# Kernel tuning notes

Measured on AMD Instinct MI355X. Metric: run time of the kernel, lower is better.

The kernel has to match this reference:

```python
import jax, jax.numpy as jnp
import numpy as np

N_NODES = 10000
N_EDGES = 160000
C = 16        # num_feature_channels
C2 = 8        # output channels per irrep per head (C/2)
HID = 64      # radial_network_hidden_units
NH = 2        # num_attention_heads
NG = 16       # graphs in batch
F_IN = 64     # num_features
F_OUT = 32    # number_of_output_features
HEAD_TYPES = ("normal", "inverse")  # invariant_dictionary
IRREP_SLICES = ((0, 1), (1, 4), (4, 9))  # l=0,1,2 blocks of the SH dim


def _sph_harm(r):
    """Component-normalized real spherical harmonics l=0..2 for unit vectors r [E,3] -> [E,9]."""
    x, y, z = r[:, 0], r[:, 1], r[:, 2]
    c3 = 1.7320508   # sqrt(3)
    c15 = 3.8729833  # sqrt(15)
    l0 = jnp.ones_like(x)[:, None]
    l1 = c3 * r
    l2 = jnp.stack([
        c15 * x * y,
        c15 * y * z,
        1.1180340 * (2.0 * z * z - x * x - y * y),  # sqrt(5)/2
        c15 * x * z,
        1.9364917 * (x * x - y * y),                 # sqrt(15)/2
    ], axis=-1)
    return jnp.concatenate([l0, l1, l2], axis=-1)


def setup_inputs() -> dict:
    key = jax.random.key(0)
    ks = jax.random.split(key, 16)
    node_features = jax.random.normal(ks[0], (N_NODES, F_IN), jnp.float32)
    pos = jax.random.normal(ks[1], (N_NODES, 3), jnp.float32)
    src = jax.random.randint(ks[2], (N_EDGES,), 0, N_NODES)
    off = jax.random.randint(ks[3], (N_EDGES,), 1, N_NODES)  # avoid self-loops (d=0)
    tgt = (src + off) % N_NODES
    edge_index = jnp.stack([src, tgt], axis=0)
    batch = jnp.sort(jax.random.randint(ks[4], (N_NODES,), 0, NG))
    s = lambda k, shape, fan: (jax.random.normal(k, shape, jnp.float32) / np.sqrt(fan)).astype(jnp.float32)
    return dict(
        node_features=node_features, pos=pos,
        W_embed=s(ks[5], (F_IN, C), F_IN), b_embed=jnp.zeros((C,), jnp.float32),
        Wq=s(ks[6], (NH, C, C), C), Wk=s(ks[7], (NH, C, C), C),
        W1=s(ks[8], (NH, 1, HID), 1), b1=jnp.zeros((NH, HID), jnp.float32),
        Wa=s(ks[9], (NH, HID), HID), Wv=s(ks[10], (NH, HID, C * 3), HID),
        Wo=s(ks[11], (NH, 3, C, C2), C),
        Wproj=s(ks[12], (NH * C2, F_OUT), NH * C2), bproj=jnp.zeros((F_OUT,), jnp.float32),
        edge_index=edge_index, batch=batch,
    )


def _forward(node_features, pos, W_embed, b_embed, Wq, Wk, W1, b1, Wa, Wv, Wo,
             Wproj, bproj, edge_index, batch):
    src, tgt = edge_index[0], edge_index[1]
    rel = pos[tgt] - pos[src]                       # [E,3]
    dist = jnp.linalg.norm(rel, axis=-1, keepdims=True)  # [E,1]
    rhat = rel / dist
    Y = _sph_harm(rhat)                             # [E,9]
    x = node_features @ W_embed + b_embed          # [N,C] scalar (0e) features
    xs = x[src]                                     # [E,C]
    inv_sqrt_c = 1.0 / np.sqrt(C)
    head_outs = []
    for h in range(NH):
        d_feat = dist if HEAD_TYPES[h] == "normal" else dist ** -2  # [E,1]
        hid = jax.nn.relu(d_feat @ W1[h] + b1[h])   # [E,HID] radial network
        att_bias = hid @ Wa[h]                      # [E]
        wv = (hid @ Wv[h]).reshape(-1, C, 3)        # [E,C,3] per-(channel,l) radial weights
        q = x @ Wq[h]
        k = x @ Wk[h]
        logit = jnp.sum(q[tgt] * k[src], axis=-1) * inv_sqrt_c + att_bias  # [E]
        # segment softmax over incoming edges of each target node
        m = jax.ops.segment_max(logit, tgt, num_segments=N_NODES)
        e = jnp.exp(logit - m[tgt])
        z = jax.ops.segment_sum(e, tgt, num_segments=N_NODES)
        alpha = e / z[tgt]                          # [E]
        # expand per-l weights to per-m: dims (1,3,5)
        wv_m = jnp.repeat(wv, np.array([1, 3, 5]), axis=2, total_repeat_length=9)  # [E,C,9]
        msg = (alpha[:, None, None] * wv_m) * xs[:, :, None] * Y[:, None, :]       # [E,C,9]
        node_out = jax.ops.segment_sum(msg, tgt, num_segments=N_NODES)             # [N,C,9]
        parts = [jnp.einsum('ncm,co->nom', node_out[:, :, s0:s1], Wo[h, li]).reshape(N_NODES, -1)
                 for li, (s0, s1) in enumerate(IRREP_SLICES)]
        head_outs.append(jnp.concatenate(parts, axis=-1))  # [N, C2*9]
    feat = jnp.concatenate(head_outs, axis=-1)              # [N, NH*C2*9]
    pooled = jax.ops.segment_sum(feat, batch, num_segments=NG)  # [NG, NH*C2*9]
    # equivariant Linear -> F_OUT x 0e: only scalar (l=0) components map to scalars
    blk = C2 * 9
    scal = jnp.concatenate([pooled[:, h * blk: h * blk + C2] for h in range(NH)], axis=-1)  # [NG, NH*C2]
    return scal @ Wproj + bproj                             # [NG, F_OUT]


def reference(node_features, pos, W_embed, b_embed, Wq, Wk, W1, b1, Wa, Wv, Wo,
              Wproj, bproj, edge_index, batch):
    return _forward(node_features, pos, W_embed, b_embed, Wq, Wk, W1, b1, Wa, Wv,
                    Wo, Wproj, bproj, edge_index, batch)
```

## Files before the change

### kernel.cpp

```cpp
#include <hip/hip_runtime.h>
#include <math.h>

#define NN 10000
#define NE 160000
#define CAP 96
#define TPH 2432
#define AATT_OFF 64
#define BATT_OFF 132
#define A_OFF 200
#define B_OFF 1312


__device__ __forceinline__ unsigned bf16pack2(float a, float b) {
    unsigned ua = __float_as_uint(a);
    unsigned ub = __float_as_uint(b);
    ua = ua + 0x7fffu + ((ua >> 16) & 1u);
    ub = ub + 0x7fffu + ((ub >> 16) & 1u);
    return (ua >> 16) | (ub & 0xffff0000u);
}

__global__ __launch_bounds__(256) void k_xqk(const float* __restrict__ nf,
        const float* __restrict__ We, const float* __restrict__ be,
        const float* __restrict__ Wq, const float* __restrict__ Wk,
        const float* __restrict__ W1, const float* __restrict__ b1,
        const float* __restrict__ Wa, const float* __restrict__ Wv,
        float* __restrict__ x, float* __restrict__ q, float* __restrict__ k,
        int* __restrict__ zeroReg, float* __restrict__ tab) {
    int t = threadIdx.x;
    int gid = blockIdx.x * 256 + t;
    if (gid < 10256) zeroReg[gid] = 0;
    __shared__ float sWe[64 * 16];
    __shared__ float sWq[2 * 16 * 16];
    __shared__ float sWk[2 * 16 * 16];
    __shared__ float sNF[16 * 64];
    __shared__ float sX[16 * 16];
    __shared__ float sT[2][64], sDA[2][64], sDB[2][64], sIA[2][64], sIB[2][64];
    __shared__ float sW[2][64][17];
    __shared__ short sOrd[2][64];
    for (int i = t; i < 1024; i += 256) sWe[i] = We[i];
    for (int i = t; i < 512; i += 256) { sWq[i] = Wq[i]; sWk[i] = Wk[i]; }
    int nodeBase = blockIdx.x * 16;
    for (int i = t; i < 1024; i += 256) {
        int n = nodeBase + (i >> 6);
        sNF[i] = (n < NN) ? nf[n * 64 + (i & 63)] : 0.0f;
    }
    __syncthreads();
    int ln = t >> 4, c = t & 15;
    int n = nodeBase + ln;
    float acc = be[c];
    #pragma unroll 16
    for (int j = 0; j < 64; ++j) acc = fmaf(sNF[ln * 64 + j], sWe[j * 16 + c], acc);
    sX[ln * 16 + c] = acc;
    __syncthreads();
    if (n < NN) {
        x[n * 16 + c] = acc;
        #pragma unroll
        for (int h = 0; h < 2; ++h) {
            float aq = 0.0f, ak = 0.0f;
            #pragma unroll
            for (int j = 0; j < 16; ++j) {
                float xv = sX[ln * 16 + j];
                aq = fmaf(xv, sWq[(h * 16 + j) * 16 + c], aq);
                ak = fmaf(xv, sWk[(h * 16 + j) * 16 + c], ak);
            }
            q[(n * 2 + h) * 16 + c] = aq;
            k[(n * 2 + h) * 16 + c] = ak;
        }
    }
    if (blockIdx.x == 0) {
        if (t < 128) {
            int h = t >> 6, j = t & 63;
            float a = W1[h * 64 + j], b = b1[h * 64 + j];
            float da = 0.0f, db = 0.0f, ia = 0.0f, ib = 0.0f, th;
            if (a > 0.0f)      { th = -b / a; da = a;  db = b; }
            else if (a < 0.0f) { th = -b / a; da = -a; db = -b; ia = a; ib = b; }
            else               { th = INFINITY; if (b > 0.0f) ib = b; }
            sT[h][j] = th; sDA[h][j] = da; sDB[h][j] = db; sIA[h][j] = ia; sIB[h][j] = ib;
        }
        for (int i = t; i < 2 * 64 * 17; i += 256) {
            int h = i / 1088, r = i % 1088, j = r / 17, cc = r % 17;
            sW[h][j][cc] = (cc < 16) ? Wv[(h * 64 + j) * 48 + 3 * cc] : Wa[h * 64 + j];
        }
        __syncthreads();
        if (t < 128) {
            int h = t >> 6, j = t & 63;
            float tj = sT[h][j];
            int r = 0;
            #pragma unroll 16
            for (int kk = 0; kk < 64; ++kk) {
                float tk = sT[h][kk];
                r += (tk < tj || (tk == tj && kk < j)) ? 1 : 0;
            }
            sOrd[h][r] = (short)j;
            tab[h * TPH + r] = tj;
        }
        __syncthreads();
        if (t < 34) {
            int h = t / 17, cc = t % 17;
            float A = 0.0f, B = 0.0f;
            #pragma unroll 8
            for (int j = 0; j < 64; ++j) {
                float w = sW[h][j][cc];
                A = fmaf(sIA[h][j], w, A);
                B = fmaf(sIB[h][j], w, B);
            }
            float* pa; float* pb; int stride;
            if (cc == 16) { pa = tab + h * TPH + AATT_OFF; pb = tab + h * TPH + BATT_OFF; stride = 1; }
            else          { pa = tab + h * TPH + A_OFF + cc; pb = tab + h * TPH + B_OFF + cc; stride = 17; }
            pa[0] = A; pb[0] = B;
            #pragma unroll 8
            for (int sg = 1; sg <= 64; ++sg) {
                int u = sOrd[h][sg - 1];
                float w = sW[h][u][cc];
                A = fmaf(sDA[h][u], w, A);
                B = fmaf(sDB[h][u], w, B);
                pa[sg * stride] = A;
                pb[sg * stride] = B;
            }
        }
    }
}

__global__ __launch_bounds__(256) void k_edge(const float* __restrict__ pos,
        const int* __restrict__ ei,
        const float* __restrict__ q, const float* __restrict__ k,
        const float* __restrict__ Wo, const float* __restrict__ x,
        const float* __restrict__ tab, int* __restrict__ deg,
        float* __restrict__ lgp, uint4* __restrict__ gb) {
    __shared__ float sTab[2 * TPH];
    int tid = threadIdx.x;
    for (int i = tid; i < 2 * TPH; i += 256) sTab[i] = tab[i];
    __syncthreads();
    int e = blockIdx.x * 256 + tid;
    if (e >= NE) return;
    int s = ei[e], t = ei[NE + e];
    int p = atomicAdd(&deg[t], 1);
    bool ok = (p < CAP);
    size_t slot = (size_t)t * CAP + p;
    float dx = pos[t * 3 + 0] - pos[s * 3 + 0];
    float dy = pos[t * 3 + 1] - pos[s * 3 + 1];
    float dz = pos[t * 3 + 2] - pos[s * 3 + 2];
    float d = sqrtf(dx * dx + dy * dy + dz * dz);
    float fh2[2] = { d, 1.0f / (d * d) };
    const float4* xp = (const float4*)(x + (size_t)s * 16);
    float4 xs0 = xp[0], xs1 = xp[1], xs2 = xp[2], xs3 = xp[3];
    float xf[16] = { xs0.x, xs0.y, xs0.z, xs0.w, xs1.x, xs1.y, xs1.z, xs1.w,
                     xs2.x, xs2.y, xs2.z, xs2.w, xs3.x, xs3.y, xs3.z, xs3.w };
    float L2v[2];
    #pragma unroll
    for (int h = 0; h < 2; ++h) {
        const float4* qt = (const float4*)(q + (size_t)t * 32 + h * 16);
        const float4* ks = (const float4*)(k + (size_t)s * 32 + h * 16);
        float4 a0 = qt[0], a1 = qt[1], a2 = qt[2], a3 = qt[3];
        float4 b0 = ks[0], c1 = ks[1], c2 = ks[2], c3 = ks[3];
        float dot = a0.x * b0.x + a0.y * b0.y + a0.z * b0.z + a0.w * b0.w
                  + a1.x * c1.x + a1.y * c1.y + a1.z * c1.z + a1.w * c1.w
                  + a2.x * c2.x + a2.y * c2.y + a2.z * c2.z + a2.w * c2.w
                  + a3.x * c3.x + a3.y * c3.y + a3.z * c3.z + a3.w * c3.w;
        float f = fh2[h];
        const float* tb = sTab + h * TPH;
        int sg = 0;
        #pragma unroll
        for (int st = 32; st >= 1; st >>= 1)
            if (tb[sg + st - 1] < f) sg += st;
        if (tb[sg] < f) ++sg;
        float att = fmaf(tb[AATT_OFF + sg], f, tb[BATT_OFF + sg]);
        L2v[h] = fmaf(dot, 0.25f, att);
        const float* Ab = tb + A_OFF + sg * 17;
        const float* Bb = tb + B_OFF + sg * 17;
        const float* wob = Wo + h * 384;
        float g[8];
        #pragma unroll
        for (int o = 0; o < 8; ++o) g[o] = 0.0f;
        #pragma unroll
        for (int c = 0; c < 16; ++c) {
            float axc = fmaf(Ab[c], f, Bb[c]) * xf[c];
            #pragma unroll
            for (int o = 0; o < 8; ++o) g[o] = fmaf(axc, wob[c * 8 + o], g[o]);
        }
        if (ok) {
            gb[slot * 2 + h] = make_uint4(bf16pack2(g[0], g[1]), bf16pack2(g[2], g[3]),
                                          bf16pack2(g[4], g[5]), bf16pack2(g[6], g[7]));
        }
    }
    if (ok) *(float2*)(lgp + slot * 2) = make_float2(L2v[0], L2v[1]);
}

__global__ __launch_bounds__(256) void k_gather(const int* __restrict__ deg,
        const float* __restrict__ lgp, const unsigned* __restrict__ gb,
        float* __restrict__ feat) {
    int t0 = threadIdx.x;
    int wv = t0 >> 6;
    int lane = t0 & 63;
    int pid = blockIdx.x * 4 + wv;
    int n = pid >> 1, h = pid & 1;
    int dg = min(deg[n], CAP);
    int g = lane >> 2, p = lane & 3;
    float m = -INFINITY, z = 0.0f, u0 = 0.0f, u1 = 0.0f;
    const float* lgb = lgp + (size_t)n * (CAP * 2) + h;
    const unsigned* gbb = gb + (size_t)n * (CAP * 8) + h * 4 + p;
    for (int i = g; i < dg; i += 16) {
        float L = lgb[i * 2];
        unsigned wbits = gbb[(size_t)i * 8];
        float ga = __uint_as_float(wbits << 16);
        float gbv = __uint_as_float(wbits & 0xffff0000u);
        float nm = fmaxf(m, L);
        float sc = (m > -INFINITY) ? __expf(m - nm) : 0.0f;
        float w  = __expf(L - nm);
        u0 = fmaf(u0, sc, w * ga);
        u1 = fmaf(u1, sc, w * gbv);
        z  = fmaf(z, sc, w);
        m = nm;
    }
    #pragma unroll
    for (int off = 4; off <= 32; off <<= 1) {
        float mo = __shfl_xor(m, off, 64);
        float zo = __shfl_xor(z, off, 64);
        float a0o = __shfl_xor(u0, off, 64);
        float a1o = __shfl_xor(u1, off, 64);
        float nm = fmaxf(m, mo);
        float a = (m  > -INFINITY) ? __expf(m  - nm) : 0.0f;
        float b = (mo > -INFINITY) ? __expf(mo - nm) : 0.0f;
        u0 = u0 * a + a0o * b;
        u1 = u1 * a + a1o * b;
        z  = z * a + zo * b;
        m = nm;
    }
    if (lane < 4) {
        float inv = (z > 0.0f) ? 1.0f / z : 0.0f;
        *(float2*)(feat + n * 16 + h * 8 + p * 2) = make_float2(u0 * inv, u1 * inv);
    }
}

__global__ __launch_bounds__(256) void k_pool(const float* __restrict__ feat,
        const int* __restrict__ batch, float* __restrict__ pooled) {
    __shared__ float sP[256];
    int t = threadIdx.x;
    sP[t] = 0.0f;
    __syncthreads();
    int tid = blockIdx.x * 256 + t;
    int c = tid & 15, seg = tid >> 4;
    int n0 = seg * 16, n1 = min(n0 + 16, NN);
    float run = 0.0f;
    int curg = -1;
    for (int n = n0; n < n1; ++n) {
        int gg = batch[n];
        if (gg != curg) {
            if (curg >= 0) atomicAdd(&sP[curg * 16 + c], run);
            run = 0.0f; curg = gg;
        }
        run += feat[n * 16 + c];
    }
    if (curg >= 0) atomicAdd(&sP[curg * 16 + c], run);
    __syncthreads();
    atomicAdd(&pooled[t], sP[t]);
}

__global__ __launch_bounds__(512) void k_final(const float* __restrict__ pooled,
        const float* __restrict__ Wproj, const float* __restrict__ bproj,
        float* __restrict__ out) {
    int t = threadIdx.x;
    int g = t >> 5, fo = t & 31;
    float acc = bproj[fo];
    #pragma unroll
    for (int j = 0; j < 16; ++j) acc = fmaf(pooled[g * 16 + j], Wproj[j * 32 + fo], acc);
    out[g * 32 + fo] = acc;
}

extern "C" void kernel_launch(void* const* d_in, const int* in_sizes, int n_in,
                              void* d_out, int out_size, void* d_ws, size_t ws_size,
                              hipStream_t stream) {
    const float* nf    = (const float*)d_in[0];
    const float* pos   = (const float*)d_in[1];
    const float* We    = (const float*)d_in[2];
    const float* be    = (const float*)d_in[3];
    const float* Wq    = (const float*)d_in[4];
    const float* Wk    = (const float*)d_in[5];
    const float* W1    = (const float*)d_in[6];
    const float* b1    = (const float*)d_in[7];
    const float* Wa    = (const float*)d_in[8];
    const float* Wv    = (const float*)d_in[9];
    const float* Wo    = (const float*)d_in[10];
    const float* Wproj = (const float*)d_in[11];
    const float* bproj = (const float*)d_in[12];
    const int*   ei    = (const int*)d_in[13];
    const int*   batch = (const int*)d_in[14];
    float* out = (float*)d_out;
    (void)in_sizes; (void)n_in; (void)out_size; (void)ws_size;

    float* ws     = (float*)d_ws;
    float* x      = ws;
    float* q      = x + 160000;
    float* k      = q + 320000;
    float* feat   = k + 320000;
    float* pooled = feat + 160000;
    int*   deg    = (int*)(pooled + 256);
    float* tab    = (float*)(deg + 10000);
    float* lgp    = tab + 4864;
    unsigned* gbu = (unsigned*)(lgp + (size_t)NN * CAP * 2);

    hipLaunchKernelGGL(k_xqk,    dim3(625),  dim3(256), 0, stream, nf, We, be, Wq, Wk, W1, b1, Wa, Wv, x, q, k, (int*)pooled, tab);
    hipLaunchKernelGGL(k_edge,   dim3(625),  dim3(256), 0, stream, pos, ei, q, k, Wo, x, tab, deg, lgp, (uint4*)gbu);
    hipLaunchKernelGGL(k_gather, dim3(5000), dim3(256), 0, stream, deg, lgp, gbu, feat);
    hipLaunchKernelGGL(k_pool,   dim3(40),   dim3(256), 0, stream, feat, batch, pooled);
    hipLaunchKernelGGL(k_final,  dim3(1),    dim3(512), 0, stream, pooled, Wproj, bproj, out);
}
```

Baseline: 138.9 us.

## Bin edges by target in prep, compute messages per node with online softmax

Edge binning by target now happens in the first kernel, which stores only source indices. A new per-node kernel (32 lanes per node) computes the distances, table lookups, messages and online softmax directly, then combines lanes with shuffles. This replaces the separate edge kernel that wrote bf16 messages and logits, and the gather kernel that read them back, removing a large intermediate round trip. Pool and final projection are merged using a last-block counter, the table build is parallelised with prefix sums, and the A/B rows are padded to 20 for float4 loads. In exchange, the table is now read from global memory rather than LDS, and work per wave is uneven across lanes for nodes with low degree.

```diff
diff --git a/kernel.cpp b/kernel.cpp
--- a/kernel.cpp
+++ b/kernel.cpp
@@ -4,39 +4,33 @@
 #define NN 10000
 #define NE 160000
 #define CAP 96
-#define TPH 2432
+#define TPH 2832
 #define AATT_OFF 64
 #define BATT_OFF 132
 #define A_OFF 200
-#define B_OFF 1312
-
-
-__device__ __forceinline__ unsigned bf16pack2(float a, float b) {
-    unsigned ua = __float_as_uint(a);
-    unsigned ub = __float_as_uint(b);
-    ua = ua + 0x7fffu + ((ua >> 16) & 1u);
-    ub = ub + 0x7fffu + ((ub >> 16) & 1u);
-    return (ua >> 16) | (ub & 0xffff0000u);
-}
-
-__global__ __launch_bounds__(256) void k_xqk(const float* __restrict__ nf,
+#define B_OFF 1520
+
+
+__global__ __launch_bounds__(256) void k_pre(const float* __restrict__ nf,
         const float* __restrict__ We, const float* __restrict__ be,
         const float* __restrict__ Wq, const float* __restrict__ Wk,
         const float* __restrict__ W1, const float* __restrict__ b1,
         const float* __restrict__ Wa, const float* __restrict__ Wv,
+        const int* __restrict__ ei,
         float* __restrict__ x, float* __restrict__ q, float* __restrict__ k,
-        int* __restrict__ zeroReg, float* __restrict__ tab) {
+        int* __restrict__ deg, int* __restrict__ srcBin, float* __restrict__ tab) {
     int t = threadIdx.x;
     int gid = blockIdx.x * 256 + t;
-    if (gid < 10256) zeroReg[gid] = 0;
+    {
+        int s = ei[gid], tt = ei[NE + gid];
+        int p = atomicAdd(&deg[tt], 1);
+        if (p < CAP) srcBin[tt * CAP + p] = s;
+    }
     __shared__ float sWe[64 * 16];
     __shared__ float sWq[2 * 16 * 16];
     __shared__ float sWk[2 * 16 * 16];
     __shared__ float sNF[16 * 64];
     __shared__ float sX[16 * 16];
-    __shared__ float sT[2][64], sDA[2][64], sDB[2][64], sIA[2][64], sIB[2][64];
-    __shared__ float sW[2][64][17];
-    __shared__ short sOrd[2][64];
     for (int i = t; i < 1024; i += 256) sWe[i] = We[i];
     for (int i = t; i < 512; i += 256) { sWq[i] = Wq[i]; sWk[i] = Wk[i]; }
     int nodeBase = blockIdx.x * 16;
@@ -68,6 +62,10 @@
         }
     }
     if (blockIdx.x == 0) {
+        __shared__ float sT[2][64], sDA[2][64], sDB[2][64], sIA[2][64], sIB[2][64];
+        __shared__ float sW[2][64][17];
+        __shared__ short sOrd[2][64];
+        __shared__ float sQA[2][17][4], sQB[2][17][4], sPA[2][17][4], sPB[2][17][4];
         if (t < 128) {
             int h = t >> 6, j = t & 63;
             float a = W1[h * 64 + j], b = b1[h * 64 + j];
@@ -95,145 +93,155 @@
             tab[h * TPH + r] = tj;
         }
         __syncthreads();
-        if (t < 34) {
-            int h = t / 17, cc = t % 17;
-            float A = 0.0f, B = 0.0f;
-            #pragma unroll 8
-            for (int j = 0; j < 64; ++j) {
-                float w = sW[h][j][cc];
-                A = fmaf(sIA[h][j], w, A);
-                B = fmaf(sIB[h][j], w, B);
-            }
+        int h = 0, cc = 0, qt = 0;
+        bool act = (t < 136);
+        if (act) { h = t / 68; int r = t % 68; cc = r >> 2; qt = r & 3; }
+        float qsA = 0.f, qsB = 0.f, ipA = 0.f, ipB = 0.f;
+        if (act) {
+            #pragma unroll 4
+            for (int i = 0; i < 16; ++i) {
+                int r = qt * 16 + i;
+                int u = sOrd[h][r];
+                float w = sW[h][u][cc];
+                qsA = fmaf(sDA[h][u], w, qsA);
+                qsB = fmaf(sDB[h][u], w, qsB);
+                float wj = sW[h][r][cc];
+                ipA = fmaf(sIA[h][r], wj, ipA);
+                ipB = fmaf(sIB[h][r], wj, ipB);
+            }
+            sQA[h][cc][qt] = qsA; sQB[h][cc][qt] = qsB;
+            sPA[h][cc][qt] = ipA; sPB[h][cc][qt] = ipB;
+        }
+        __syncthreads();
+        if (act) {
+            float A = sPA[h][cc][0] + sPA[h][cc][1] + sPA[h][cc][2] + sPA[h][cc][3];
+            float B = sPB[h][cc][0] + sPB[h][cc][1] + sPB[h][cc][2] + sPB[h][cc][3];
+            for (int qq = 0; qq < qt; ++qq) { A += sQA[h][cc][qq]; B += sQB[h][cc][qq]; }
             float* pa; float* pb; int stride;
             if (cc == 16) { pa = tab + h * TPH + AATT_OFF; pb = tab + h * TPH + BATT_OFF; stride = 1; }
-            else          { pa = tab + h * TPH + A_OFF + cc; pb = tab + h * TPH + B_OFF + cc; stride = 17; }
-            pa[0] = A; pb[0] = B;
-            #pragma unroll 8
-            for (int sg = 1; sg <= 64; ++sg) {
-                int u = sOrd[h][sg - 1];
+            else          { pa = tab + h * TPH + A_OFF + cc; pb = tab + h * TPH + B_OFF + cc; stride = 20; }
+            #pragma unroll 4
+            for (int i = 0; i < 16; ++i) {
+                int r = qt * 16 + i;
+                pa[r * stride] = A;
+                pb[r * stride] = B;
+                int u = sOrd[h][r];
                 float w = sW[h][u][cc];
                 A = fmaf(sDA[h][u], w, A);
                 B = fmaf(sDB[h][u], w, B);
-                pa[sg * stride] = A;
-                pb[sg * stride] = B;
-            }
+            }
+            if (qt == 3) { pa[64 * stride] = A; pb[64 * stride] = B; }
         }
     }
 }
 
-__global__ __launch_bounds__(256) void k_edge(const float* __restrict__ pos,
-        const int* __restrict__ ei,
-        const float* __restrict__ q, const float* __restrict__ k,
-        const float* __restrict__ Wo, const float* __restrict__ x,
-        const float* __restrict__ tab, int* __restrict__ deg,
-        float* __restrict__ lgp, uint4* __restrict__ gb) {
-    __shared__ float sTab[2 * TPH];
-    int tid = threadIdx.x;
-    for (int i = tid; i < 2 * TPH; i += 256) sTab[i] = tab[i];
-    __syncthreads();
-    int e = blockIdx.x * 256 + tid;
-    if (e >= NE) return;
-    int s = ei[e], t = ei[NE + e];
-    int p = atomicAdd(&deg[t], 1);
-    bool ok = (p < CAP);
-    size_t slot = (size_t)t * CAP + p;
-    float dx = pos[t * 3 + 0] - pos[s * 3 + 0];
-    float dy = pos[t * 3 + 1] - pos[s * 3 + 1];
-    float dz = pos[t * 3 + 2] - pos[s * 3 + 2];
-    float d = sqrtf(dx * dx + dy * dy + dz * dz);
-    float fh2[2] = { d, 1.0f / (d * d) };
-    const float4* xp = (const float4*)(x + (size_t)s * 16);
-    float4 xs0 = xp[0], xs1 = xp[1], xs2 = xp[2], xs3 = xp[3];
-    float xf[16] = { xs0.x, xs0.y, xs0.z, xs0.w, xs1.x, xs1.y, xs1.z, xs1.w,
-                     xs2.x, xs2.y, xs2.z, xs2.w, xs3.x, xs3.y, xs3.z, xs3.w };
-    float L2v[2];
+__global__ __launch_bounds__(256) void k_node(const float* __restrict__ pos,
+        const int* __restrict__ deg, const int* __restrict__ srcBin,
+        const float* __restrict__ q, const float* __restrict__ kk,
+        const float* __restrict__ x, const float* __restrict__ tab,
+        const float* __restrict__ Wo, float* __restrict__ feat) {
+    int t = threadIdx.x;
+    int n = blockIdx.x * 8 + (t >> 5);
+    int lane = t & 31;
+    int dg = min(deg[n], CAP);
+    float ptx = pos[n * 3 + 0], pty = pos[n * 3 + 1], ptz = pos[n * 3 + 2];
+    const float4* qp = (const float4*)(q + (size_t)n * 32);
+    float4 qv0 = qp[0], qv1 = qp[1], qv2 = qp[2], qv3 = qp[3];
+    float4 qv4 = qp[4], qv5 = qp[5], qv6 = qp[6], qv7 = qp[7];
+    float m[2] = { -INFINITY, -INFINITY };
+    float z[2] = { 0.0f, 0.0f };
+    float u[2][8];
+    #pragma unroll
+    for (int h = 0; h < 2; ++h)
+        #pragma unroll
+        for (int o = 0; o < 8; ++o) u[h][o] = 0.0f;
+    for (int slot = lane; slot < dg; slot += 32) {
+        int s = srcBin[n * CAP + slot];
+        float dx = ptx - pos[s * 3 + 0];
+        float dy = pty - pos[s * 3 + 1];
+        float dz = ptz - pos[s * 3 + 2];
+        float d = sqrtf(dx * dx + dy * dy + dz * dz);
+        const float4* xp = (const float4*)(x + (size_t)s * 16);
+        float4 xs0 = xp[0], xs1 = xp[1], xs2 = xp[2], xs3 = xp[3];
+        float Xf[16] = { xs0.x, xs0.y, xs0.z, xs0.w, xs1.x, xs1.y, xs1.z, xs1.w,
+                         xs2.x, xs2.y, xs2.z, xs2.w, xs3.x, xs3.y, xs3.z, xs3.w };
+        #pragma unroll
+        for (int h = 0; h < 2; ++h) {
+            const float4* kp = (const float4*)(kk + (size_t)s * 32 + h * 16);
+            float4 k0 = kp[0], k1 = kp[1], k2 = kp[2], k3 = kp[3];
+            float4 a0 = h ? qv4 : qv0, a1 = h ? qv5 : qv1;
+            float4 a2 = h ? qv6 : qv2, a3 = h ? qv7 : qv3;
+            float dot = a0.x * k0.x + a0.y * k0.y + a0.z * k0.z + a0.w * k0.w
+                      + a1.x * k1.x + a1.y * k1.y + a1.z * k1.z + a1.w * k1.w
+                      + a2.x * k2.x + a2.y * k2.y + a2.z * k2.z + a2.w * k2.w
+                      + a3.x * k3.x + a3.y * k3.y + a3.z * k3.z + a3.w * k3.w;
+            float f = h ? 1.0f / (d * d) : d;
+            const float* tb = tab + h * TPH;
+            int sg = 0;
+            #pragma unroll
+            for (int st = 32; st >= 1; st >>= 1)
+                if (tb[sg + st - 1] < f) sg += st;
+            if (tb[sg] < f) ++sg;
+            float att = fmaf(tb[AATT_OFF + sg], f, tb[BATT_OFF + sg]);
+            float L = fmaf(dot, 0.25f, att);
+            const float4* Ar = (const float4*)(tb + A_OFF + sg * 20);
+            const float4* Br = (const float4*)(tb + B_OFF + sg * 20);
+            float4 A0 = Ar[0], A1 = Ar[1], A2 = Ar[2], A3 = Ar[3];
+            float4 B0 = Br[0], B1 = Br[1], B2 = Br[2], B3 = Br[3];
+            float Af[16] = { A0.x, A0.y, A0.z, A0.w, A1.x, A1.y, A1.z, A1.w,
+                             A2.x, A2.y, A2.z, A2.w, A3.x, A3.y, A3.z, A3.w };
+            float Bf[16] = { B0.x, B0.y, B0.z, B0.w, B1.x, B1.y, B1.z, B1.w,
+                             B2.x, B2.y, B2.z, B2.w, B3.x, B3.y, B3.z, B3.w };
+            float g[8];
+            #pragma unroll
+            for (int o = 0; o < 8; ++o) g[o] = 0.0f;
+            const float* wob = Wo + h * 384;
+            #pragma unroll
+            for (int c = 0; c < 16; ++c) {
+                float ax = fmaf(Af[c], f, Bf[c]) * Xf[c];
+                #pragma unroll
+                for (int o = 0; o < 8; ++o) g[o] = fmaf(ax, wob[c * 8 + o], g[o]);
+            }
+            float nm = fmaxf(m[h], L);
+            float sc = (m[h] > -INFINITY) ? __expf(m[h] - nm) : 0.0f;
+            float w = __expf(L - nm);
+            #pragma unroll
+            for (int o = 0; o < 8; ++o) u[h][o] = fmaf(u[h][o], sc, w * g[o]);
+            z[h] = fmaf(z[h], sc, w);
+            m[h] = nm;
+        }
+    }
     #pragma unroll
     for (int h = 0; h < 2; ++h) {
-        const float4* qt = (const float4*)(q + (size_t)t * 32 + h * 16);
-        const float4* ks = (const float4*)(k + (size_t)s * 32 + h * 16);
-        float4 a0 = qt[0], a1 = qt[1], a2 = qt[2], a3 = qt[3];
-        float4 b0 = ks[0], c1 = ks[1], c2 = ks[2], c3 = ks[3];
-        float dot = a0.x * b0.x + a0.y * b0.y + a0.z * b0.z + a0.w * b0.w
-                  + a1.x * c1.x + a1.y * c1.y + a1.z * c1.z + a1.w * c1.w
-                  + a2.x * c2.x + a2.y * c2.y + a2.z * c2.z + a2.w * c2.w
-                  + a3.x * c3.x + a3.y * c3.y + a3.z * c3.z + a3.w * c3.w;
-        float f = fh2[h];
-        const float* tb = sTab + h * TPH;
-        int sg = 0;
-        #pragma unroll
-        for (int st = 32; st >= 1; st >>= 1)
-            if (tb[sg + st - 1] < f) sg += st;
-        if (tb[sg] < f) ++sg;
-        float att = fmaf(tb[AATT_OFF + sg], f, tb[BATT_OFF + sg]);
-        L2v[h] = fmaf(dot, 0.25f, att);
-        const float* Ab = tb + A_OFF + sg * 17;
-        const float* Bb = tb + B_OFF + sg * 17;
-        const float* wob = Wo + h * 384;
-        float g[8];
-        #pragma unroll
-        for (int o = 0; o < 8; ++o) g[o] = 0.0f;
-        #pragma unroll
-        for (int c = 0; c < 16; ++c) {
-            float axc = fmaf(Ab[c], f, Bb[c]) * xf[c];
-            #pragma unroll
-            for (int o = 0; o < 8; ++o) g[o] = fmaf(axc, wob[c * 8 + o], g[o]);
-        }
-        if (ok) {
-            gb[slot * 2 + h] = make_uint4(bf16pack2(g[0], g[1]), bf16pack2(g[2], g[3]),
-                                          bf16pack2(g[4], g[5]), bf16pack2(g[6], g[7]));
-        }
-    }
-    if (ok) *(float2*)(lgp + slot * 2) = make_float2(L2v[0], L2v[1]);
+        float mh = m[h], zh = z[h];
+        #pragma unroll
+        for (int off = 1; off <= 16; off <<= 1) {
+            float mo = __shfl_xor(mh, off, 64);
+            float zo = __shfl_xor(zh, off, 64);
+            float uo[8];
+            #pragma unroll
+            for (int o = 0; o < 8; ++o) uo[o] = __shfl_xor(u[h][o], off, 64);
+            float nm = fmaxf(mh, mo);
+            float a = (mh > -INFINITY) ? __expf(mh - nm) : 0.0f;
+            float b = (mo > -INFINITY) ? __expf(mo - nm) : 0.0f;
+            #pragma unroll
+            for (int o = 0; o < 8; ++o) u[h][o] = u[h][o] * a + uo[o] * b;
+            zh = zh * a + zo * b;
+            mh = nm;
+        }
+        if (lane == 0) {
+            float inv = (zh > 0.0f) ? 1.0f / zh : 0.0f;
+            float4* fp = (float4*)(feat + (size_t)n * 16 + h * 8);
+            fp[0] = make_float4(u[h][0] * inv, u[h][1] * inv, u[h][2] * inv, u[h][3] * inv);
+            fp[1] = make_float4(u[h][4] * inv, u[h][5] * inv, u[h][6] * inv, u[h][7] * inv);
+        }
+    }
 }
 
-__global__ __launch_bounds__(256) void k_gather(const int* __restrict__ deg,
-        const float* __restrict__ lgp, const unsigned* __restrict__ gb,
-        float* __restrict__ feat) {
-    int t0 = threadIdx.x;
-    int wv = t0 >> 6;
-    int lane = t0 & 63;
-    int pid = blockIdx.x * 4 + wv;
-    int n = pid >> 1, h = pid & 1;
-    int dg = min(deg[n], CAP);
-    int g = lane >> 2, p = lane & 3;
-    float m = -INFINITY, z = 0.0f, u0 = 0.0f, u1 = 0.0f;
-    const float* lgb = lgp + (size_t)n * (CAP * 2) + h;
-    const unsigned* gbb = gb + (size_t)n * (CAP * 8) + h * 4 + p;
-    for (int i = g; i < dg; i += 16) {
-        float L = lgb[i * 2];
-        unsigned wbits = gbb[(size_t)i * 8];
-        float ga = __uint_as_float(wbits << 16);
-        float gbv = __uint_as_float(wbits & 0xffff0000u);
-        float nm = fmaxf(m, L);
-        float sc = (m > -INFINITY) ? __expf(m - nm) : 0.0f;
-        float w  = __expf(L - nm);
-        u0 = fmaf(u0, sc, w * ga);
-        u1 = fmaf(u1, sc, w * gbv);
-        z  = fmaf(z, sc, w);
-        m = nm;
-    }
-    #pragma unroll
-    for (int off = 4; off <= 32; off <<= 1) {
-        float mo = __shfl_xor(m, off, 64);
-        float zo = __shfl_xor(z, off, 64);
-        float a0o = __shfl_xor(u0, off, 64);
-        float a1o = __shfl_xor(u1, off, 64);
-        float nm = fmaxf(m, mo);
-        float a = (m  > -INFINITY) ? __expf(m  - nm) : 0.0f;
-        float b = (mo > -INFINITY) ? __expf(mo - nm) : 0.0f;
-        u0 = u0 * a + a0o * b;
-        u1 = u1 * a + a1o * b;
-        z  = z * a + zo * b;
-        m = nm;
-    }
-    if (lane < 4) {
-        float inv = (z > 0.0f) ? 1.0f / z : 0.0f;
-        *(float2*)(feat + n * 16 + h * 8 + p * 2) = make_float2(u0 * inv, u1 * inv);
-    }
-}
-
-__global__ __launch_bounds__(256) void k_pool(const float* __restrict__ feat,
-        const int* __restrict__ batch, float* __restrict__ pooled) {
+__global__ __launch_bounds__(256) void k_poolfinal(const float* __restrict__ feat,
+        const int* __restrict__ batch, float* __restrict__ pooled,
+        int* __restrict__ done, const float* __restrict__ Wproj,
+        const float* __restrict__ bproj, float* __restrict__ out) {
     __shared__ float sP[256];
     int t = threadIdx.x;
     sP[t] = 0.0f;
@@ -254,17 +262,22 @@
     if (curg >= 0) atomicAdd(&sP[curg * 16 + c], run);
     __syncthreads();
     atomicAdd(&pooled[t], sP[t]);
-}
-
-__global__ __launch_bounds__(512) void k_final(const float* __restrict__ pooled,
-        const float* __restrict__ Wproj, const float* __restrict__ bproj,
-        float* __restrict__ out) {
-    int t = threadIdx.x;
-    int g = t >> 5, fo = t & 31;
-    float acc = bproj[fo];
-    #pragma unroll
-    for (int j = 0; j < 16; ++j) acc = fmaf(pooled[g * 16 + j], Wproj[j * 32 + fo], acc);
-    out[g * 32 + fo] = acc;
+    __threadfence();
+    __shared__ int lastBlk;
+    if (t == 0) lastBlk = (atomicAdd(done, 1) == 39) ? 1 : 0;
+    __syncthreads();
+    if (!lastBlk) return;
+    __threadfence();
+    __shared__ float sPool[256];
+    sPool[t] = atomicAdd(&pooled[t], 0.0f);
+    __syncthreads();
+    for (int i = t; i < 512; i += 256) {
+        int g = i >> 5, fo = i & 31;
+        float acc = bproj[fo];
+        #pragma unroll
+        for (int j = 0; j < 16; ++j) acc = fmaf(sPool[g * 16 + j], Wproj[j * 32 + fo], acc);
+        out[g * 32 + fo] = acc;
+    }
 }
 
 extern "C" void kernel_launch(void* const* d_in, const int* in_sizes, int n_in,
@@ -295,13 +308,15 @@
     float* feat   = k + 320000;
     float* pooled = feat + 160000;
     int*   deg    = (int*)(pooled + 256);
-    float* tab    = (float*)(deg + 10000);
-    float* lgp    = tab + 4864;
-    unsigned* gbu = (unsigned*)(lgp + (size_t)NN * CAP * 2);
-
-    hipLaunchKernelGGL(k_xqk,    dim3(625),  dim3(256), 0, stream, nf, We, be, Wq, Wk, W1, b1, Wa, Wv, x, q, k, (int*)pooled, tab);
-    hipLaunchKernelGGL(k_edge,   dim3(625),  dim3(256), 0, stream, pos, ei, q, k, Wo, x, tab, deg, lgp, (uint4*)gbu);
-    hipLaunchKernelGGL(k_gather, dim3(5000), dim3(256), 0, stream, deg, lgp, gbu, feat);
-    hipLaunchKernelGGL(k_pool,   dim3(40),   dim3(256), 0, stream, feat, batch, pooled);
-    hipLaunchKernelGGL(k_final,  dim3(1),    dim3(512), 0, stream, pooled, Wproj, bproj, out);
+    int*   done   = deg + 10000;
+    int*   srcBin = done + 16;
+    float* tab    = (float*)(srcBin + 960000);
+
+    hipMemsetAsync(pooled, 0, (256 + 10000 + 16) * sizeof(int), stream);
+    hipLaunchKernelGGL(k_pre,       dim3(625),  dim3(256), 0, stream,
+                       nf, We, be, Wq, Wk, W1, b1, Wa, Wv, ei, x, q, k, deg, srcBin, tab);
+    hipLaunchKernelGGL(k_node,      dim3(1250), dim3(256), 0, stream,
+                       pos, deg, srcBin, q, k, x, tab, Wo, feat);
+    hipLaunchKernelGGL(k_poolfinal, dim3(40),   dim3(256), 0, stream,
+                       feat, batch, pooled, done, Wproj, bproj, out);
 }
```

Result: no change. 138.7 us (-0.2%).
